# Kernel optimization log

Measured on AMD Instinct MI355X. Metric: run time of the kernel, lower is better.

## Reference

```python
import jax, jax.numpy as jnp
import numpy as np

H = 16  # num_heads


def setup_inputs() -> dict:
    key = jax.random.key(0)
    k1, k2, k3, k4, k5, k6 = jax.random.split(key, 6)
    B, T, K = 4, 2048, 1024
    x = jax.random.normal(k1, (B, T, K), dtype=jnp.float32)
    s = 1.0 / np.sqrt(K)
    Wq = jax.random.normal(k2, (K, K), dtype=jnp.float32) * s
    Wk = jax.random.normal(k3, (K, K), dtype=jnp.float32) * s
    Wv = jax.random.normal(k4, (K, K), dtype=jnp.float32) * s
    Wp = jax.random.normal(k5, (K, K), dtype=jnp.float32) * s
    bp = jax.random.normal(k6, (K,), dtype=jnp.float32) * 0.01
    return {"input_data": x, "Wq": Wq, "Wk": Wk, "Wv": Wv, "Wp": Wp, "bp": bp}


def reference(input_data, Wq, Wk, Wv, Wp, bp):
    B, T, K = input_data.shape
    S = K // H
    # torch Linear: y = x @ W.T
    q = (input_data @ Wq.T).reshape(B, T, H, S).transpose(0, 2, 1, 3)  # [B,H,T,S]
    k = (input_data @ Wk.T).reshape(B, T, H, S).transpose(0, 2, 1, 3)
    v = (input_data @ Wv.T).reshape(B, T, H, S).transpose(0, 2, 1, 3)
    scale = float(H) ** -0.5  # NB: original scales by num_heads**-0.5, not head_dim
    wei = jnp.einsum("bhts,bhus->bhtu", q, k) * scale  # [B,H,T,T]
    causal = jnp.tril(jnp.ones((T, T), dtype=bool))
    wei = jnp.where(causal, wei, -jnp.inf)
    wei = jax.nn.softmax(wei, axis=-1)
    out = jnp.einsum("bhtu,bhus->bhts", wei, v)  # [B,H,T,S]
    out = out.transpose(0, 2, 1, 3).reshape(B, T, K)
    return out @ Wp.T + bp
```

## Files before the change

kernel.cpp:

```cpp
#include <hip/hip_runtime.h>
#include <hip/hip_bf16.h>
#include <math.h>

typedef __bf16 bf16;
typedef __bf16 bf16x8 __attribute__((ext_vector_type(8)));
typedef float f32x4 __attribute__((ext_vector_type(4)));

#define MFMA16(a, b, c) __builtin_amdgcn_mfma_f32_16x16x32_bf16(a, b, c, 0, 0, 0)

__device__ __forceinline__ void gload16(const void* g, void* l) {
    __builtin_amdgcn_global_load_lds(
        (const __attribute__((address_space(1))) void*)g,
        (__attribute__((address_space(3))) void*)l, 16, 0, 0);
}

__global__ void cast_f32_bf16(const float* __restrict__ src, bf16* __restrict__ dst, int n8) {
    int i = blockIdx.x * blockDim.x + threadIdx.x;
    if (i >= n8) return;
    const float4* s = (const float4*)src;
    float4 v0 = s[i * 2], v1 = s[i * 2 + 1];
    bf16x8 o;
    o[0] = (bf16)v0.x; o[1] = (bf16)v0.y; o[2] = (bf16)v0.z; o[3] = (bf16)v0.w;
    o[4] = (bf16)v1.x; o[5] = (bf16)v1.y; o[6] = (bf16)v1.z; o[7] = (bf16)v1.w;
    *(bf16x8*)(dst + i * 8) = o;
}

__global__ void cast_weights(const float* __restrict__ Wq, const float* __restrict__ Wk,
                             const float* __restrict__ Wv, const float* __restrict__ Wp,
                             bf16* __restrict__ wqkv, bf16* __restrict__ wp) {
    int c = blockIdx.x * blockDim.x + threadIdx.x;
    int mat = c >> 17, loc = c & 131071;
    const float* src = (mat == 0) ? Wq : (mat == 1) ? Wk : (mat == 2) ? Wv : Wp;
    bf16* dst = (mat == 3) ? wp : (wqkv + (size_t)mat * 1048576);
    const float4* s = (const float4*)(src) + loc * 2;
    float4 v0 = s[0], v1 = s[1];
    bf16x8 o;
    o[0] = (bf16)v0.x; o[1] = (bf16)v0.y; o[2] = (bf16)v0.z; o[3] = (bf16)v0.w;
    o[4] = (bf16)v1.x; o[5] = (bf16)v1.y; o[6] = (bf16)v1.z; o[7] = (bf16)v1.w;
    *(bf16x8*)(dst + (size_t)loc * 8) = o;
}

__device__ __forceinline__ void gemm_mainloop(
    const bf16* __restrict__ A, const bf16* __restrict__ W,
    int tm, int tn, int K, bf16* As, bf16* Bs,
    f32x4 acc[4][4], int lane, int wave, int wr, int wc) {
    for (int k0 = 0; k0 < K; k0 += 64) {
#pragma unroll
        for (int it = 0; it < 4; ++it) {
            int o = it * 4096 + wave * 1024 + lane * 16;
            int L = o ^ (((o >> 7) & 7) << 4);
            int row = L >> 7, colb = L & 127;
            gload16((const char*)A + ((size_t)(tm + row) * K + k0) * 2 + colb,
                    (char*)As + it * 4096 + wave * 1024);
            gload16((const char*)W + ((size_t)(tn + row) * K + k0) * 2 + colb,
                    (char*)Bs + it * 4096 + wave * 1024);
        }
        __syncthreads();
#pragma unroll
        for (int kk = 0; kk < 64; kk += 32) {
            bf16x8 a[4], b[4];
#pragma unroll
            for (int i = 0; i < 4; ++i) {
                int row = wr * 64 + i * 16 + (lane & 15);
                int byte = (row * 128 + kk * 2 + ((lane >> 4) * 16)) ^ ((row & 7) << 4);
                a[i] = *(const bf16x8*)((const char*)As + byte);
            }
#pragma unroll
            for (int j = 0; j < 4; ++j) {
                int row = wc * 64 + j * 16 + (lane & 15);
                int byte = (row * 128 + kk * 2 + ((lane >> 4) * 16)) ^ ((row & 7) << 4);
                b[j] = *(const bf16x8*)((const char*)Bs + byte);
            }
#pragma unroll
            for (int i = 0; i < 4; ++i)
#pragma unroll
                for (int j = 0; j < 4; ++j)
                    acc[i][j] = MFMA16(a[i], b[j], acc[i][j]);
        }
        __syncthreads();
    }
}

__global__ void gemm_qkv(const bf16* __restrict__ A, const bf16* __restrict__ W,
                         bf16* __restrict__ qkv) {
    __shared__ bf16 SM[128 * 128];
    bf16* As = SM;
    bf16* Bs = SM + 8192;
    const int tid = threadIdx.x;
    const int lane = tid & 63, wave = tid >> 6;
    const int wr = wave >> 1, wc = wave & 1;
    const int l15 = lane & 15, hi = lane >> 4;
    const int tm = blockIdx.y * 128, tn = blockIdx.x * 128;
    f32x4 acc[4][4] = {};
    gemm_mainloop(A, W, tm, tn, 1024, As, Bs, acc, lane, wave, wr, wc);
    const int mat = tn >> 10;
    if (mat == 2) {
#pragma unroll
        for (int i = 0; i < 4; ++i)
#pragma unroll
            for (int r = 0; r < 4; ++r) {
                int tl = wr * 64 + i * 16 + hi * 4 + r;
#pragma unroll
                for (int j = 0; j < 4; ++j) {
                    int c = wc * 64 + j * 16 + l15;
                    int byte = (c * 256 + tl * 2) ^ ((c & 7) << 4);
                    *(bf16*)((char*)SM + byte) = (bf16)acc[i][j][r];
                }
            }
        __syncthreads();
        const int b16 = (tm >> 11) * 16, tmod = tm & 2047;
#pragma unroll
        for (int pass = 0; pass < 8; ++pass) {
            int c = (tid >> 4) + pass * 16;
            int h = ((tn + c) >> 6) & 15, s = c & 63;
            int byte = (c * 256 + (tid & 15) * 16) ^ ((c & 7) << 4);
            bf16x8 v = *(const bf16x8*)((const char*)SM + byte);
            size_t base = (size_t)(128 + b16 + h) * 131072 + (size_t)s * 2048 + tmod;
            *(bf16x8*)(qkv + base + (tid & 15) * 8) = v;
        }
    } else {
        const float scale = (mat == 0) ? 0.25f : 1.0f;
#pragma unroll
        for (int i = 0; i < 4; ++i)
#pragma unroll
            for (int r = 0; r < 4; ++r) {
                int m = tm + wr * 64 + i * 16 + hi * 4 + r;
                int b_ = m >> 11, t = m & 2047;
#pragma unroll
                for (int j = 0; j < 4; ++j) {
                    int n = tn + wc * 64 + j * 16 + l15;
                    int h = (n >> 6) & 15, s = n & 63;
                    qkv[(size_t)(mat * 64 + b_ * 16 + h) * 131072 + (size_t)t * 64 + s] =
                        (bf16)(acc[i][j][r] * scale);
                }
            }
    }
}

__global__ void gemm_out(const bf16* __restrict__ A, const bf16* __restrict__ W,
                         const float* __restrict__ bias, float* __restrict__ out) {
    __shared__ bf16 As[128 * 64];
    __shared__ bf16 Bs[128 * 64];
    const int lane = threadIdx.x & 63, wave = threadIdx.x >> 6;
    const int wr = wave >> 1, wc = wave & 1;
    const int tm = blockIdx.y * 128, tn = blockIdx.x * 128;
    f32x4 acc[4][4] = {};
    gemm_mainloop(A, W, tm, tn, 1024, As, Bs, acc, lane, wave, wr, wc);
#pragma unroll
    for (int i = 0; i < 4; ++i)
#pragma unroll
        for (int r = 0; r < 4; ++r) {
            int m = tm + wr * 64 + i * 16 + (lane >> 4) * 4 + r;
#pragma unroll
            for (int j = 0; j < 4; ++j) {
                int n = tn + wc * 64 + j * 16 + (lane & 15);
                out[(size_t)m * 1024 + n] = acc[i][j][r] + bias[n];
            }
        }
}

__global__ __launch_bounds__(256, 4)
void attn_kernel(const bf16* __restrict__ qkv, bf16* __restrict__ attn_out) {
    const int wgid = blockIdx.x;
    const int qp = (wgid >> 3) & 7;
    const int bh = ((wgid & 7) << 3) | (wgid >> 6);
    const int tid = threadIdx.x;
    const int lane = tid & 63, wave = tid >> 6;
    const int l15 = lane & 15, hi = lane >> 4;
    const bf16* Qp = qkv + (size_t)bh * 131072;
    const bf16* Kp = qkv + (size_t)(64 + bh) * 131072;
    const bf16* Vt = qkv + (size_t)(128 + bh) * 131072;

    __shared__ bf16 KsBuf[2][4096];
    __shared__ bf16 VsBuf[2][4096];
    __shared__ bf16 PsBuf[8192];

    int k_off[2], vt_off[2];
#pragma unroll
    for (int c = 0; c < 2; ++c) {
        int i = c * 256 + tid;
        int o = i * 16;
        int row = i >> 3;
        int colb = (o ^ ((row & 7) << 4)) & 127;
        k_off[c]  = row * 128  + colb;
        vt_off[c] = row * 4096 + colb;
    }

    const int b_ = bh >> 4, h = bh & 15;

    for (int pass = 0; pass < 2; ++pass) {
        const int qi = pass ? (15 - qp) : qp;
        bf16x8 qf[2][2];
#pragma unroll
        for (int rf = 0; rf < 2; ++rf) {
            int row = qi * 128 + wave * 32 + rf * 16 + l15;
#pragma unroll
            for (int ks = 0; ks < 2; ++ks)
                qf[rf][ks] = *(const bf16x8*)(Qp + (size_t)row * 64 + ks * 32 + hi * 8);
        }
        f32x4 o_acc[2][4] = {};
        float l_run[2][4] = {};

        const int nkt = 2 * qi + 2;
        __syncthreads();
#pragma unroll
        for (int c = 0; c < 2; ++c) {
            gload16((const char*)Kp + k_off[c], (char*)KsBuf[0] + c * 4096 + wave * 1024);
            gload16((const char*)Vt + vt_off[c], (char*)VsBuf[0] + c * 4096 + wave * 1024);
        }
        int cur = 0;
        for (int kt = 0; kt < nkt; ++kt) {
            __syncthreads();
            if (kt + 1 < nkt) {
                size_t kof = (size_t)(kt + 1) * 8192;
                size_t vof = (size_t)(kt + 1) * 128;
#pragma unroll
                for (int c = 0; c < 2; ++c) {
                    gload16((const char*)Kp + kof + k_off[c],
                            (char*)KsBuf[cur ^ 1] + c * 4096 + wave * 1024);
                    gload16((const char*)Vt + vof + vt_off[c],
                            (char*)VsBuf[cur ^ 1] + c * 4096 + wave * 1024);
                }
            }

            const char* Ks = (const char*)KsBuf[cur];
            const char* Vs = (const char*)VsBuf[cur];
            f32x4 sc[2][4] = {};
#pragma unroll
            for (int ks = 0; ks < 2; ++ks)
#pragma unroll
                for (int kf = 0; kf < 4; ++kf) {
                    int row = kf * 16 + l15;
                    int byte = (row * 128 + ks * 64 + hi * 16) ^ ((row & 7) << 4);
                    bf16x8 kb = *(const bf16x8*)(Ks + byte);
#pragma unroll
                    for (int rf = 0; rf < 2; ++rf)
                        sc[rf][kf] = MFMA16(qf[rf][ks], kb, sc[rf][kf]);
                }

            if (kt >= 2 * qi) {
#pragma unroll
                for (int rf = 0; rf < 2; ++rf)
#pragma unroll
                    for (int r = 0; r < 4; ++r) {
                        int row_g = qi * 128 + wave * 32 + rf * 16 + hi * 4 + r;
#pragma unroll
                        for (int kf = 0; kf < 4; ++kf) {
                            int key_g = kt * 64 + kf * 16 + l15;
                            float p = (key_g > row_g) ? 0.f : __expf(sc[rf][kf][r]);
                            sc[rf][kf][r] = p;
                            l_run[rf][r] += p;
                        }
                    }
            } else {
#pragma unroll
                for (int rf = 0; rf < 2; ++rf)
#pragma unroll
                    for (int r = 0; r < 4; ++r)
#pragma unroll
                        for (int kf = 0; kf < 4; ++kf) {
                            float p = __expf(sc[rf][kf][r]);
                            sc[rf][kf][r] = p;
                            l_run[rf][r] += p;
                        }
            }

#pragma unroll
            for (int rf = 0; rf < 2; ++rf)
#pragma unroll
                for (int kf = 0; kf < 4; ++kf)
#pragma unroll
                    for (int r = 0; r < 4; ++r) {
                        int row = wave * 32 + rf * 16 + hi * 4 + r;
                        int byte = (row * 128 + (kf * 16 + l15) * 2) ^ (((row >> 1) & 7) << 4);
                        *(bf16*)((char*)PsBuf + byte) = (bf16)sc[rf][kf][r];
                    }
            asm volatile("s_waitcnt lgkmcnt(0)" ::: "memory");
            __builtin_amdgcn_sched_barrier(0);

#pragma unroll
            for (int ks = 0; ks < 2; ++ks) {
                bf16x8 pa[2];
#pragma unroll
                for (int rf = 0; rf < 2; ++rf) {
                    int prow = wave * 32 + rf * 16 + l15;
                    int pbyte = (prow * 128 + ks * 64 + hi * 16) ^ (((prow >> 1) & 7) << 4);
                    pa[rf] = *(const bf16x8*)((const char*)PsBuf + pbyte);
                }
#pragma unroll
                for (int sf = 0; sf < 4; ++sf) {
                    int srow = sf * 16 + l15;
                    int vbyte = (srow * 128 + ks * 64 + hi * 16) ^ ((srow & 7) << 4);
                    bf16x8 vb = *(const bf16x8*)(Vs + vbyte);
#pragma unroll
                    for (int rf = 0; rf < 2; ++rf)
                        o_acc[rf][sf] = MFMA16(pa[rf], vb, o_acc[rf][sf]);
                }
            }
            cur ^= 1;
        }

#pragma unroll
        for (int rf = 0; rf < 2; ++rf)
#pragma unroll
            for (int r = 0; r < 4; ++r) {
                float l = l_run[rf][r];
#pragma unroll
                for (int mk = 1; mk < 16; mk <<= 1)
                    l += __shfl_xor(l, mk, 64);
                float inv = 1.0f / l;
                int t = qi * 128 + wave * 32 + rf * 16 + hi * 4 + r;
                size_t base = ((size_t)(b_ * 2048 + t)) * 1024 + h * 64;
#pragma unroll
                for (int sf = 0; sf < 4; ++sf)
                    attn_out[base + sf * 16 + l15] = (bf16)(o_acc[rf][sf][r] * inv);
            }
    }
}

extern "C" void kernel_launch(void* const* d_in, const int* in_sizes, int n_in,
                              void* d_out, int out_size, void* d_ws, size_t ws_size,
                              hipStream_t stream) {
    const float* x  = (const float*)d_in[0];
    const float* Wq = (const float*)d_in[1];
    const float* Wk = (const float*)d_in[2];
    const float* Wv = (const float*)d_in[3];
    const float* Wp = (const float*)d_in[4];
    const float* bp = (const float*)d_in[5];
    float* out = (float*)d_out;

    char* ws = (char*)d_ws;
    bf16* x_bf   = (bf16*)(ws);
    bf16* wqkv   = (bf16*)(ws + 16777216);
    bf16* wp_bf  = (bf16*)(ws + 23068672);
    bf16* qkv    = (bf16*)(ws + 25165824);
    bf16* attn_b = (bf16*)(ws + 75497472);

    cast_f32_bf16<<<dim3(4096), 256, 0, stream>>>(x, x_bf, 8192 * 1024 / 8);
    cast_weights<<<dim3(2048), 256, 0, stream>>>(Wq, Wk, Wv, Wp, wqkv, wp_bf);

    gemm_qkv<<<dim3(24, 64), 256, 0, stream>>>(x_bf, wqkv, qkv);
    attn_kernel<<<dim3(512), 256, 0, stream>>>(qkv, attn_b);
    gemm_out<<<dim3(8, 64), 256, 0, stream>>>(attn_b, wp_bf, bp, out);
}
```

Baseline: 160.1 us.

## Split attention into one query tile per block and drop K/V double buffering

The attention kernel now launches 1024 blocks, each handling one 128-row query tile, with the heaviest tiles scheduled first. Previously 512 blocks each processed a paired light and heavy tile in two passes. K/V shared-memory double buffering is removed in favour of a single buffer with load-then-sync each iteration. This halves LDS per block and may raise occupancy and improve load balance, but global-load latency is no longer overlapped with compute within a block.

Result: slower. 432.1 us (+169.9%).

```diff
diff --git a/kernel.cpp b/kernel.cpp
--- a/kernel.cpp
+++ b/kernel.cpp
@@ -162,8 +162,8 @@
 __global__ __launch_bounds__(256, 4)
 void attn_kernel(const bf16* __restrict__ qkv, bf16* __restrict__ attn_out) {
     const int wgid = blockIdx.x;
-    const int qp = (wgid >> 3) & 7;
-    const int bh = ((wgid & 7) << 3) | (wgid >> 6);
+    const int qi = 15 - ((wgid >> 3) & 15);
+    const int bh = ((wgid & 7) << 3) | (wgid >> 7);
     const int tid = threadIdx.x;
     const int lane = tid & 63, wave = tid >> 6;
     const int l15 = lane & 15, hi = lane >> 4;
@@ -171,8 +171,8 @@
     const bf16* Kp = qkv + (size_t)(64 + bh) * 131072;
     const bf16* Vt = qkv + (size_t)(128 + bh) * 131072;
 
-    __shared__ bf16 KsBuf[2][4096];
-    __shared__ bf16 VsBuf[2][4096];
+    __shared__ bf16 KsBuf[4096];
+    __shared__ bf16 VsBuf[4096];
     __shared__ bf16 PsBuf[8192];
 
     int k_off[2], vt_off[2];
@@ -188,134 +188,118 @@
 
     const int b_ = bh >> 4, h = bh & 15;
 
-    for (int pass = 0; pass < 2; ++pass) {
-        const int qi = pass ? (15 - qp) : qp;
-        bf16x8 qf[2][2];
-#pragma unroll
-        for (int rf = 0; rf < 2; ++rf) {
-            int row = qi * 128 + wave * 32 + rf * 16 + l15;
-#pragma unroll
-            for (int ks = 0; ks < 2; ++ks)
-                qf[rf][ks] = *(const bf16x8*)(Qp + (size_t)row * 64 + ks * 32 + hi * 8);
-        }
-        f32x4 o_acc[2][4] = {};
-        float l_run[2][4] = {};
-
-        const int nkt = 2 * qi + 2;
+    bf16x8 qf[2][2];
+#pragma unroll
+    for (int rf = 0; rf < 2; ++rf) {
+        int row = qi * 128 + wave * 32 + rf * 16 + l15;
+#pragma unroll
+        for (int ks = 0; ks < 2; ++ks)
+            qf[rf][ks] = *(const bf16x8*)(Qp + (size_t)row * 64 + ks * 32 + hi * 8);
+    }
+    f32x4 o_acc[2][4] = {};
+    float l_run[2][4] = {};
+
+    const int nkt = 2 * qi + 2;
+    for (int kt = 0; kt < nkt; ++kt) {
         __syncthreads();
 #pragma unroll
         for (int c = 0; c < 2; ++c) {
-            gload16((const char*)Kp + k_off[c], (char*)KsBuf[0] + c * 4096 + wave * 1024);
-            gload16((const char*)Vt + vt_off[c], (char*)VsBuf[0] + c * 4096 + wave * 1024);
-        }
-        int cur = 0;
-        for (int kt = 0; kt < nkt; ++kt) {
-            __syncthreads();
-            if (kt + 1 < nkt) {
-                size_t kof = (size_t)(kt + 1) * 8192;
-                size_t vof = (size_t)(kt + 1) * 128;
-#pragma unroll
-                for (int c = 0; c < 2; ++c) {
-                    gload16((const char*)Kp + kof + k_off[c],
-                            (char*)KsBuf[cur ^ 1] + c * 4096 + wave * 1024);
-                    gload16((const char*)Vt + vof + vt_off[c],
-                            (char*)VsBuf[cur ^ 1] + c * 4096 + wave * 1024);
+            gload16((const char*)Kp + (size_t)kt * 8192 + k_off[c],
+                    (char*)KsBuf + c * 4096 + wave * 1024);
+            gload16((const char*)Vt + (size_t)kt * 128 + vt_off[c],
+                    (char*)VsBuf + c * 4096 + wave * 1024);
+        }
+        __syncthreads();
+
+        f32x4 sc[2][4] = {};
+#pragma unroll
+        for (int ks = 0; ks < 2; ++ks)
+#pragma unroll
+            for (int kf = 0; kf < 4; ++kf) {
+                int row = kf * 16 + l15;
+                int byte = (row * 128 + ks * 64 + hi * 16) ^ ((row & 7) << 4);
+                bf16x8 kb = *(const bf16x8*)((const char*)KsBuf + byte);
+#pragma unroll
+                for (int rf = 0; rf < 2; ++rf)
+                    sc[rf][kf] = MFMA16(qf[rf][ks], kb, sc[rf][kf]);
+            }
+
+        if (kt >= 2 * qi) {
+#pragma unroll
+            for (int rf = 0; rf < 2; ++rf)
+#pragma unroll
+                for (int r = 0; r < 4; ++r) {
+                    int row_g = qi * 128 + wave * 32 + rf * 16 + hi * 4 + r;
+#pragma unroll
+                    for (int kf = 0; kf < 4; ++kf) {
+                        int key_g = kt * 64 + kf * 16 + l15;
+                        float p = (key_g > row_g) ? 0.f : __expf(sc[rf][kf][r]);
+                        sc[rf][kf][r] = p;
+                        l_run[rf][r] += p;
+                    }
                 }
-            }
-
-            const char* Ks = (const char*)KsBuf[cur];
-            const char* Vs = (const char*)VsBuf[cur];
-            f32x4 sc[2][4] = {};
-#pragma unroll
-            for (int ks = 0; ks < 2; ++ks)
-#pragma unroll
-                for (int kf = 0; kf < 4; ++kf) {
-                    int row = kf * 16 + l15;
-                    int byte = (row * 128 + ks * 64 + hi * 16) ^ ((row & 7) << 4);
-                    bf16x8 kb = *(const bf16x8*)(Ks + byte);
-#pragma unroll
-                    for (int rf = 0; rf < 2; ++rf)
-                        sc[rf][kf] = MFMA16(qf[rf][ks], kb, sc[rf][kf]);
+        } else {
+#pragma unroll
+            for (int rf = 0; rf < 2; ++rf)
+#pragma unroll
+                for (int r = 0; r < 4; ++r)
+#pragma unroll
+                    for (int kf = 0; kf < 4; ++kf) {
+                        float p = __expf(sc[rf][kf][r]);
+                        sc[rf][kf][r] = p;
+                        l_run[rf][r] += p;
+                    }
+        }
+
+#pragma unroll
+        for (int rf = 0; rf < 2; ++rf)
+#pragma unroll
+            for (int kf = 0; kf < 4; ++kf)
+#pragma unroll
+                for (int r = 0; r < 4; ++r) {
+                    int row = wave * 32 + rf * 16 + hi * 4 + r;
+                    int byte = (row * 128 + (kf * 16 + l15) * 2) ^ (((row >> 1) & 7) << 4);
+                    *(bf16*)((char*)PsBuf + byte) = (bf16)sc[rf][kf][r];
                 }
-
-            if (kt >= 2 * qi) {
+        asm volatile("s_waitcnt lgkmcnt(0)" ::: "memory");
+        __builtin_amdgcn_sched_barrier(0);
+
+#pragma unroll
+        for (int ks = 0; ks < 2; ++ks) {
+            bf16x8 pa[2];
+#pragma unroll
+            for (int rf = 0; rf < 2; ++rf) {
+                int prow = wave * 32 + rf * 16 + l15;
+                int pbyte = (prow * 128 + ks * 64 + hi * 16) ^ (((prow >> 1) & 7) << 4);
+                pa[rf] = *(const bf16x8*)((const char*)PsBuf + pbyte);
+            }
+#pragma unroll
+            for (int sf = 0; sf < 4; ++sf) {
+                int srow = sf * 16 + l15;
+                int vbyte = (srow * 128 + ks * 64 + hi * 16) ^ ((srow & 7) << 4);
+                bf16x8 vb = *(const bf16x8*)((const char*)VsBuf + vbyte);
 #pragma unroll
                 for (int rf = 0; rf < 2; ++rf)
-#pragma unroll
-                    for (int r = 0; r < 4; ++r) {
-                        int row_g = qi * 128 + wave * 32 + rf * 16 + hi * 4 + r;
-#pragma unroll
-                        for (int kf = 0; kf < 4; ++kf) {
-                            int key_g = kt * 64 + kf * 16 + l15;
-                            float p = (key_g > row_g) ? 0.f : __expf(sc[rf][kf][r]);
-                            sc[rf][kf][r] = p;
-                            l_run[rf][r] += p;
-                        }
-                    }
-            } else {
-#pragma unroll
-                for (int rf = 0; rf < 2; ++rf)
-#pragma unroll
-                    for (int r = 0; r < 4; ++r)
-#pragma unroll
-                        for (int kf = 0; kf < 4; ++kf) {
-                            float p = __expf(sc[rf][kf][r]);
-                            sc[rf][kf][r] = p;
-                            l_run[rf][r] += p;
-                        }
-            }
-
-#pragma unroll
-            for (int rf = 0; rf < 2; ++rf)
-#pragma unroll
-                for (int kf = 0; kf < 4; ++kf)
-#pragma unroll
-                    for (int r = 0; r < 4; ++r) {
-                        int row = wave * 32 + rf * 16 + hi * 4 + r;
-                        int byte = (row * 128 + (kf * 16 + l15) * 2) ^ (((row >> 1) & 7) << 4);
-                        *(bf16*)((char*)PsBuf + byte) = (bf16)sc[rf][kf][r];
-                    }
-            asm volatile("s_waitcnt lgkmcnt(0)" ::: "memory");
-            __builtin_amdgcn_sched_barrier(0);
-
-#pragma unroll
-            for (int ks = 0; ks < 2; ++ks) {
-                bf16x8 pa[2];
-#pragma unroll
-                for (int rf = 0; rf < 2; ++rf) {
-                    int prow = wave * 32 + rf * 16 + l15;
-                    int pbyte = (prow * 128 + ks * 64 + hi * 16) ^ (((prow >> 1) & 7) << 4);
-                    pa[rf] = *(const bf16x8*)((const char*)PsBuf + pbyte);
-                }
-#pragma unroll
-                for (int sf = 0; sf < 4; ++sf) {
-                    int srow = sf * 16 + l15;
-                    int vbyte = (srow * 128 + ks * 64 + hi * 16) ^ ((srow & 7) << 4);
-                    bf16x8 vb = *(const bf16x8*)(Vs + vbyte);
-#pragma unroll
-                    for (int rf = 0; rf < 2; ++rf)
-                        o_acc[rf][sf] = MFMA16(pa[rf], vb, o_acc[rf][sf]);
-                }
-            }
-            cur ^= 1;
-        }
-
-#pragma unroll
-        for (int rf = 0; rf < 2; ++rf)
-#pragma unroll
-            for (int r = 0; r < 4; ++r) {
-                float l = l_run[rf][r];
-#pragma unroll
-                for (int mk = 1; mk < 16; mk <<= 1)
-                    l += __shfl_xor(l, mk, 64);
-                float inv = 1.0f / l;
-                int t = qi * 128 + wave * 32 + rf * 16 + hi * 4 + r;
-                size_t base = ((size_t)(b_ * 2048 + t)) * 1024 + h * 64;
-#pragma unroll
-                for (int sf = 0; sf < 4; ++sf)
-                    attn_out[base + sf * 16 + l15] = (bf16)(o_acc[rf][sf][r] * inv);
-            }
-    }
+                    o_acc[rf][sf] = MFMA16(pa[rf], vb, o_acc[rf][sf]);
+            }
+        }
+    }
+
+#pragma unroll
+    for (int rf = 0; rf < 2; ++rf)
+#pragma unroll
+        for (int r = 0; r < 4; ++r) {
+            float l = l_run[rf][r];
+#pragma unroll
+            for (int mk = 1; mk < 16; mk <<= 1)
+                l += __shfl_xor(l, mk, 64);
+            float inv = 1.0f / l;
+            int t = qi * 128 + wave * 32 + rf * 16 + hi * 4 + r;
+            size_t base = ((size_t)(b_ * 2048 + t)) * 1024 + h * 64;
+#pragma unroll
+            for (int sf = 0; sf < 4; ++sf)
+                attn_out[base + sf * 16 + l15] = (bf16)(o_acc[rf][sf][r] * inv);
+        }
 }
 
 extern "C" void kernel_launch(void* const* d_in, const int* in_sizes, int n_in,
@@ -340,6 +324,6 @@
     cast_weights<<<dim3(2048), 256, 0, stream>>>(Wq, Wk, Wv, Wp, wqkv, wp_bf);
 
     gemm_qkv<<<dim3(24, 64), 256, 0, stream>>>(x_bf, wqkv, qkv);
-    attn_kernel<<<dim3(512), 256, 0, stream>>>(qkv, attn_b);
+    attn_kernel<<<dim3(1024), 256, 0, stream>>>(qkv, attn_b);
     gemm_out<<<dim3(8, 64), 256, 0, stream>>>(attn_b, wp_bf, bp, out);
 }
```
